# Optimization experiments

Measured on AMD Instinct MI355X. Metric: run time of the kernel, lower is better.

The kernel has to match this reference:

```python
import jax, jax.numpy as jnp
import numpy as np

COST_CLASS = 1.0
COST_POINT = 1.0


def _linear_sum_assignment(cost):
    """Pure-numpy Jonker-Volgenant / Hungarian (e-maxx formulation).
    Emulates scipy.optimize.linear_sum_assignment for a dense float cost matrix.
    Returns (row_ind, col_ind) with row_ind sorted ascending.
    """
    cost = np.asarray(cost, dtype=np.float64)
    transposed = cost.shape[0] > cost.shape[1]
    if transposed:
        cost = cost.T
    n, m = cost.shape  # n <= m
    INF = np.inf
    u = np.zeros(n + 1)
    v = np.zeros(m + 1)
    p = np.zeros(m + 1, dtype=np.int64)  # p[j] = row (1-indexed) matched to col j
    for i in range(1, n + 1):
        p[0] = i
        j0 = 0
        minv = np.full(m + 1, INF)
        way = np.zeros(m + 1, dtype=np.int64)
        used = np.zeros(m + 1, dtype=bool)
        while True:
            used[j0] = True
            i0 = p[j0]
            cur = cost[i0 - 1, :] - u[i0] - v[1:]
            free = ~used[1:]
            upd = free & (cur < minv[1:])
            minv[1:][upd] = cur[upd]
            way[1:][upd] = j0
            masked = np.where(free, minv[1:], INF)
            j1 = int(np.argmin(masked)) + 1
            delta = masked[j1 - 1]
            u[p[used]] += delta
            v[used] -= delta
            minv[1:][free] -= delta
            j0 = j1
            if p[j0] == 0:
                break
        while j0 != 0:
            j1 = way[j0]
            p[j0] = p[j1]
            j0 = j1
    ans = np.zeros(n, dtype=np.int64)  # ans[row] = col
    for j in range(1, m + 1):
        if p[j] > 0:
            ans[p[j] - 1] = j - 1
    if transposed:
        # rows of the original matrix are ans values; sort by original row index
        order = np.argsort(ans)
        return ans[order], np.arange(n, dtype=np.int64)[order]
    return np.arange(n, dtype=np.int64), ans


def _cost_matrix(pred_logits, pred_points, tgt_labels, tgt_points):
    bs, Q, C = pred_logits.shape
    T = tgt_labels.shape[1]
    out_prob = jax.nn.softmax(pred_logits.reshape(bs * Q, C), axis=-1)   # [bs*Q, C]
    out_points = pred_points.reshape(bs * Q, -1)                          # [bs*Q, 2]
    tgt_ids = tgt_labels.reshape(-1)                                      # [bs*T]
    tgt_pts = tgt_points.reshape(bs * T, -1).astype(jnp.float32)          # [bs*T, 2]
    cost_class = -out_prob[:, tgt_ids]                                    # [bs*Q, bs*T]
    # L1 cdist
    cost_point = jnp.sum(jnp.abs(out_points[:, None, :] - tgt_pts[None, :, :]), axis=-1)
    Cfull = COST_POINT * cost_point + COST_CLASS * cost_class             # [bs*Q, bs*T]
    # per-batch diagonal blocks (what the scipy split selects): [bs, Q, T]
    C4 = Cfull.reshape(bs, Q, bs, T)
    Cb = C4[jnp.arange(bs), :, jnp.arange(bs), :]
    return Cb


def setup_inputs() -> dict:
    key = jax.random.key(0)
    k1, k2, k3, k4 = jax.random.split(key, 4)
    bs, Q, C, T = 16, 1024, 92, 128
    return {
        "pred_logits": jax.random.normal(k1, (bs, Q, C), dtype=jnp.float32),
        "pred_points": jax.random.uniform(k2, (bs, Q, 2), dtype=jnp.float32),
        "tgt_labels": jax.random.randint(k3, (bs, T), 0, C, dtype=jnp.int64),
        "tgt_points": jax.random.uniform(k4, (bs, T, 2), dtype=jnp.float32),
    }


def reference(pred_logits, pred_points, tgt_labels, tgt_points):
    Cb = _cost_matrix(pred_logits, pred_points, tgt_labels, tgt_points)   # [bs, Q, T]
    Cnp = np.asarray(jax.device_get(Cb))
    rows, cols = [], []
    for b in range(Cnp.shape[0]):  # structural loop over batch for the assignment
        r, c = _linear_sum_assignment(Cnp[b])
        rows.append(r)
        cols.append(c)
    row_idx = jnp.asarray(np.stack(rows))  # [bs, T] selected query indices (sorted)
    col_idx = jnp.asarray(np.stack(cols))  # [bs, T] matched target indices
    return Cb, row_idx, col_idx
```

## Files before the change

### kernel.cpp

```cpp
#include <hip/hip_runtime.h>
#include <hip/hip_bf16.h>
#include <math.h>

#define BS 16
#define Q 1024
#define CC 92
#define T 128
#define M 1024
#define NR 128
#define NQB 16

__global__ __launch_bounds__(256) void prep_kernel(
    const float* __restrict__ logits,
    const float* __restrict__ ppts,
    const int*   __restrict__ tlab,
    const float* __restrict__ tpts,
    float* __restrict__ Cb,
    float* __restrict__ CbT,
    unsigned long long* __restrict__ part)
{
    const int blk = blockIdx.x;
    const int b   = blk & 15;
    const int qb  = blk >> 4;
    const int q0  = qb * 64;
    const int tid = threadIdx.x;
    const int lane = tid & 63;

    __shared__ float lg[64 * CC];
    __shared__ float tile[128][68];
    __shared__ float tx_sh[T], ty_sh[T];
    __shared__ int   lab_sh[T];
    __shared__ float mx_sh[64], inv_sh[64], px_sh[64], py_sh[64];

    if (tid < T) {
        lab_sh[tid] = tlab[b * T + tid];
        tx_sh[tid]  = tpts[(b * T + tid) * 2 + 0];
        ty_sh[tid]  = tpts[(b * T + tid) * 2 + 1];
    }
    if (tid < 64) {
        px_sh[tid] = ppts[((size_t)b * Q + q0 + tid) * 2 + 0];
        py_sh[tid] = ppts[((size_t)b * Q + q0 + tid) * 2 + 1];
    }
    const float* lbase = logits + ((size_t)b * Q + q0) * CC;
    for (int idx = tid; idx < 64 * CC; idx += 256) lg[idx] = lbase[idx];
    __syncthreads();

    {
        const int w = tid >> 6;
        for (int s = 0; s < 16; ++s) {
            const int ql = w * 16 + s;
            const float* c = &lg[ql * CC];
            float l0 = c[lane];
            float l1 = (lane + 64 < CC) ? c[lane + 64] : -INFINITY;
            float mx = fmaxf(l0, l1);
            #pragma unroll
            for (int off = 32; off > 0; off >>= 1)
                mx = fmaxf(mx, __shfl_down(mx, off));
            mx = __shfl(mx, 0);
            float es = expf(l0 - mx) + ((lane + 64 < CC) ? expf(l1 - mx) : 0.0f);
            #pragma unroll
            for (int off = 32; off > 0; off >>= 1) es += __shfl_down(es, off);
            es = __shfl(es, 0);
            if (lane == 0) { mx_sh[ql] = mx; inv_sh[ql] = 1.0f / es; }
        }
    }
    __syncthreads();

    {
        const int ql = tid >> 2;
        const int tc = tid & 3;
        const float px = px_sh[ql], py = py_sh[ql];
        const float mx = mx_sh[ql], inv = inv_sh[ql];
        const float* lgq = &lg[ql * CC];
        float* cbrow = Cb + ((size_t)b * Q + q0 + ql) * T + tc * 32;
        #pragma unroll
        for (int k = 0; k < 8; ++k) {
            float4 o;
            #pragma unroll
            for (int e = 0; e < 4; ++e) {
                const int t = tc * 32 + 4 * k + e;
                const int labv = lab_sh[t];
                float prob = expf(lgq[labv] - mx) * inv;
                float cp   = fabsf(px - tx_sh[t]) + fabsf(py - ty_sh[t]);
                float val  = cp - prob;
                (&o.x)[e] = val;
                tile[t][ql] = val;
            }
            ((float4*)cbrow)[k] = o;
        }
    }
    __syncthreads();

    {
        const int rg = tid >> 4;
        const int c4 = tid & 15;
        #pragma unroll
        for (int it = 0; it < 8; ++it) {
            const int t = it * 16 + rg;
            float4 v = *(const float4*)&tile[t][4 * c4];
            *(float4*)(CbT + ((size_t)b * NR + t) * Q + q0 + 4 * c4) = v;

            unsigned long long bk = ~0ull;
            const float* vf = (const float*)&v;
            #pragma unroll
            for (int e = 0; e < 4; ++e) {
                unsigned bits = __float_as_uint(vf[e]);
                unsigned mono = (bits & 0x80000000u) ? ~bits
                                                     : (bits | 0x80000000u);
                const int j = q0 + 4 * c4 + e;
                unsigned long long key =
                    ((unsigned long long)mono << 10) | (unsigned)j;
                bk = (key < bk) ? key : bk;
            }
            #pragma unroll
            for (int off = 1; off < 16; off <<= 1) {
                unsigned long long ok = __shfl_xor(bk, off);
                bk = (ok < bk) ? ok : bk;
            }
            if (c4 == 0) part[((size_t)b * NQB + qb) * NR + t] = bk;
        }
    }
}

__global__ __launch_bounds__(256) void cost_kernel(
    const float* __restrict__ logits, const float* __restrict__ ppts,
    const int* __restrict__ tlab, const float* __restrict__ tpts,
    float* __restrict__ Cb)
{
    const int blk  = blockIdx.x;
    const int b    = blk >> 8;
    const int wave = threadIdx.x >> 6;
    const int lane = threadIdx.x & 63;
    const int q    = (blk & 255) * 4 + wave;

    __shared__ float tx_sh[T], ty_sh[T];
    __shared__ int   lab_sh[T];
    __shared__ float logit_sh[4][CC];

    if (threadIdx.x < T) {
        lab_sh[threadIdx.x] = tlab[b * T + threadIdx.x];
        tx_sh[threadIdx.x]  = tpts[(b * T + threadIdx.x) * 2 + 0];
        ty_sh[threadIdx.x]  = tpts[(b * T + threadIdx.x) * 2 + 1];
    }
    const float* lrow = logits + ((size_t)b * Q + q) * CC;
    float l0 = lrow[lane];
    float l1 = (lane + 64 < CC) ? lrow[lane + 64] : -INFINITY;
    logit_sh[wave][lane] = l0;
    if (lane + 64 < CC) logit_sh[wave][lane + 64] = l1;

    float mx = fmaxf(l0, l1);
    #pragma unroll
    for (int off = 32; off > 0; off >>= 1) mx = fmaxf(mx, __shfl_down(mx, off));
    mx = __shfl(mx, 0);
    float es = expf(l0 - mx) + ((lane + 64 < CC) ? expf(l1 - mx) : 0.0f);
    #pragma unroll
    for (int off = 32; off > 0; off >>= 1) es += __shfl_down(es, off);
    es = __shfl(es, 0);
    const float inv = 1.0f / es;
    const float px = ppts[((size_t)b * Q + q) * 2 + 0];
    const float py = ppts[((size_t)b * Q + q) * 2 + 1];
    __syncthreads();
    float* outrow = Cb + ((size_t)b * Q + q) * T;
    #pragma unroll
    for (int t = lane; t < T; t += 64) {
        int   labv = lab_sh[t];
        float prob = expf(logit_sh[wave][labv] - mx) * inv;
        float cp   = fabsf(px - tx_sh[t]) + fabsf(py - ty_sh[t]);
        outrow[t]  = cp - prob;
    }
}

#define DPP_UMIN_STEP(x, ctrl)                                              \
    {                                                                       \
        unsigned _t = (unsigned)__builtin_amdgcn_update_dpp(                \
            (int)(x), (int)(x), (ctrl), 0xF, 0xF, false);                   \
        (x) = ((x) < _t) ? (x) : _t;                                        \
    }

#define DPP_UMIN_REDUCE(x)                                                  \
    DPP_UMIN_STEP(x, 0x111); DPP_UMIN_STEP(x, 0x112);                       \
    DPP_UMIN_STEP(x, 0x114); DPP_UMIN_STEP(x, 0x118);                       \
    DPP_UMIN_STEP(x, 0x142); DPP_UMIN_STEP(x, 0x143);

#define DPP_UMIN2_STEP(x1, x2, ctrl)                                        \
    {                                                                       \
        unsigned _t1 = (unsigned)__builtin_amdgcn_update_dpp(               \
            (int)(x1), (int)(x1), (ctrl), 0xF, 0xF, false);                 \
        unsigned _t2 = (unsigned)__builtin_amdgcn_update_dpp(               \
            (int)(x2), (int)(x2), (ctrl), 0xF, 0xF, false);                 \
        unsigned _hi = ((x1) > _t1) ? (x1) : _t1;                           \
        unsigned _lo2 = ((x2) < _t2) ? (x2) : _t2;                          \
        (x1) = ((x1) < _t1) ? (x1) : _t1;                                   \
        (x2) = (_hi < _lo2) ? _hi : _lo2;                                   \
    }

#define DPP_UMIN2_REDUCE(x1, x2)                                            \
    DPP_UMIN2_STEP(x1, x2, 0x111); DPP_UMIN2_STEP(x1, x2, 0x112);           \
    DPP_UMIN2_STEP(x1, x2, 0x114); DPP_UMIN2_STEP(x1, x2, 0x118);           \
    DPP_UMIN2_STEP(x1, x2, 0x142); DPP_UMIN2_STEP(x1, x2, 0x143);

__device__ __forceinline__ unsigned mono_enc(float f) {
    unsigned b = __float_as_uint(f);
    return (b & 0x80000000u) ? ~b : (b | 0x80000000u);
}
__device__ __forceinline__ float mono_dec(unsigned m) {
    unsigned b = (m & 0x80000000u) ? (m ^ 0x80000000u) : ~m;
    return __uint_as_float(b);
}

template<int USET>
__global__ __launch_bounds__(64) void solve_kernel(
    const float* __restrict__ Cb,
    const float* __restrict__ CbT,
    const unsigned long long* __restrict__ part,
    float* __restrict__ out_rows,
    float* __restrict__ out_cols)
{
    const int b    = blockIdx.x;
    const int lane = threadIdx.x;

    __shared__ int    row4col[M];
    __shared__ int    col4row[NR];
    __shared__ float  u_sh[NR];
    __shared__ int    path_lds[M];
    __shared__ int    SRr[NR];
    __shared__ float  SRd[NR];
    __shared__ int    minj_sh[NR];
    __shared__ int    claim[M];

    const float* CbB  = Cb  + (size_t)b * Q * T;
    const float* CbTB = CbT + (size_t)b * NR * Q;

    for (int j = lane; j < M;  j += 64) { row4col[j] = -1; claim[j] = 0x7fffffff; }
    for (int i = lane; i < NR; i += 64) col4row[i] = -1;

    if (part) {
        #pragma unroll
        for (int r2 = 0; r2 < 2; ++r2) {
            const int r = lane + 64 * r2;
            const unsigned long long* pr = part + (size_t)b * NQB * NR + r;
            unsigned long long k = pr[0];
            #pragma unroll
            for (int i = 1; i < NQB; ++i) {
                unsigned long long o = pr[(size_t)i * NR];
                k = (o < k) ? o : k;
            }
            minj_sh[r] = (int)(k & 1023u);
            u_sh[r] = mono_dec((unsigned)(k >> 10));
        }
    } else {
        for (int i = lane; i < NR; i += 64) { minj_sh[i] = -1; u_sh[i] = 0.0f; }
    }
    __syncthreads();

    if (part) {
        #pragma unroll
        for (int r2 = 0; r2 < 2; ++r2) {
            const int r = lane + 64 * r2;
            atomicMin(&claim[minj_sh[r]], r);
        }
        __syncthreads();
        #pragma unroll
        for (int r2 = 0; r2 < 2; ++r2) {
            const int r = lane + 64 * r2;
            const int mj = minj_sh[r];
            if (claim[mj] == r) { col4row[r] = mj; row4col[mj] = r; }
        }
        __syncthreads();
    }

    const float FINF = INFINITY;
    float v_[16], dist_[16];
    #pragma unroll
    for (int k = 0; k < 16; ++k) v_[k] = 0.0f;

    {
        unsigned long long am0 = ~__ballot(col4row[lane] >= 0);
        unsigned long long am1 = ~__ballot(col4row[lane + 64] >= 0);
        for (int half = 0; half < 2; ++half) {
            unsigned long long mask = half ? am1 : am0;
            while (mask) {
                int cur = __ffsll(mask) - 1 + 64 * half;
                mask &= mask - 1;

                for (int step = 0; step < 48; ++step) {
                    const float ucur = u_sh[cur];

                    float4 c4[4];
                    if (USET) {
                        const float4* row =
                            (const float4*)(CbTB + (size_t)cur * Q);
                        #pragma unroll
                        for (int g = 0; g < 4; ++g) c4[g] = row[lane + 64 * g];
                    } else {
                        const float* col = CbB + cur;
                        #pragma unroll
                        for (int g = 0; g < 4; ++g) {
                            float* cf = (float*)&c4[g];
                            #pragma unroll
                            for (int e = 0; e < 4; ++e)
                                cf[e] = col[(size_t)(256*g + 4*lane + e) * T];
                        }
                    }

                    float m1l = FINF, m2l = FINF; int j1l = 0;
                    #pragma unroll
                    for (int g = 0; g < 4; ++g) {
                        const float* cf = (const float*)&c4[g];
                        #pragma unroll
                        for (int e = 0; e < 4; ++e) {
                            const int k = 4 * g + e;
                            const int j = 256 * g + 4 * lane + e;
                            float r = cf[e] - ucur - v_[k];
                            if (r < m1l) { m2l = m1l; m1l = r; j1l = j; }
                            else if (r < m2l) { m2l = r; }
                        }
                    }

                    const int cand = row4col[j1l];

                    const unsigned lm1 = mono_enc(m1l);
                    unsigned e1 = lm1;
                    unsigned e2 = mono_enc(m2l);
                    DPP_UMIN2_REDUCE(e1, e2);
                    const unsigned g1 =
                        (unsigned)__builtin_amdgcn_readlane((int)e1, 63);
                    const unsigned g2 =
                        (unsigned)__builtin_amdgcn_readlane((int)e2, 63);
                    const float m1 = mono_dec(g1);
                    const float m2 = mono_dec(g2);

                    const unsigned long long bm = __ballot(lm1 == g1);
                    const int winner = __ffsll(bm) - 1;
                    const int j1   = __builtin_amdgcn_readlane(j1l, winner);
                    const int disp = __builtin_amdgcn_readlane(cand, winner);

                    if (lane == 0) u_sh[cur] = ucur + m2;
                    if (((j1 >> 2) & 63) == lane) {
                        const int k = ((j1 >> 8) << 2) | (j1 & 3);
                        v_[k] -= (m2 - m1);
                    }

                    if (lane == 0) {
                        row4col[j1]  = cur;
                        col4row[cur] = j1;
                        if (disp >= 0) col4row[disp] = -1;
                    }
                    if (disp < 0) { cur = -1; break; }
                    cur = disp;
                }
            }
        }
    }

    unsigned long long um0 = ~__ballot(col4row[lane] >= 0);
    unsigned long long um1 = ~__ballot(col4row[lane + 64] >= 0);

    for (int half = 0; half < 2; ++half) {
        unsigned long long mask = half ? um1 : um0;
        while (mask) {
            const int curRow = __ffsll(mask) - 1 + 64 * half;
            mask &= mask - 1;

            #pragma unroll
            for (int k = 0; k < 16; ++k) dist_[k] = FINF;
            unsigned used  = 0;
            float    minVal = 0.0f;
            int      i_s  = curRow;
            int      sink = -1;
            int      cnt  = 0;

            for (int guard = 0; guard <= M; ++guard) {
                const float ui = u_sh[i_s];
                const float s  = minVal - ui;

                float4 c4[4];
                if (USET) {
                    const float4* row = (const float4*)(CbTB + (size_t)i_s * Q);
                    #pragma unroll
                    for (int g = 0; g < 4; ++g) c4[g] = row[lane + 64 * g];
                } else {
                    const float* col = CbB + i_s;
                    #pragma unroll
                    for (int g = 0; g < 4; ++g) {
                        float* cf = (float*)&c4[g];
                        #pragma unroll
                        for (int e = 0; e < 4; ++e)
                            cf[e] = col[(size_t)(256 * g + 4 * lane + e) * T];
                    }
                }

                float lmin = FINF; int lidx = 0;
                #pragma unroll
                for (int g = 0; g < 4; ++g) {
                    const float* cf = (const float*)&c4[g];
                    #pragma unroll
                    for (int e = 0; e < 4; ++e) {
                        const int k = 4 * g + e;
                        const int j = 256 * g + 4 * lane + e;
                        const bool fr = ((used >> k) & 1u) == 0u;
                        float r = s + cf[e] - v_[k];
                        if (fr && r < dist_[k]) {
                            dist_[k] = r;
                            path_lds[256 * g + 64 * e + lane] = i_s;
                        }
                        float a = fr ? dist_[k] : FINF;
                        if (a < lmin) { lmin = a; lidx = j; }
                    }
                }

                const int cand = row4col[lidx];

                unsigned lmono = mono_enc(lmin);
                unsigned rmin = lmono;
                DPP_UMIN_REDUCE(rmin);
                const unsigned gmin =
                    (unsigned)__builtin_amdgcn_readlane((int)rmin, 63);

                const unsigned long long bmask = __ballot(lmono == gmin);
                const int winner = __ffsll(bmask) - 1;

                minVal = __uint_as_float(
                    (unsigned)__builtin_amdgcn_readlane(
                        (int)__float_as_uint(lmin), winner));
                const int jstar = __builtin_amdgcn_readlane(lidx, winner);

                if (((jstar >> 2) & 63) == lane)
                    used |= (1u << (((jstar >> 8) << 2) | (jstar & 3)));

                const int ra = __builtin_amdgcn_readlane(cand, winner);
                if (ra == -1) { sink = jstar; break; }
                if (lane == 0 && cnt < NR) { SRr[cnt] = ra; SRd[cnt] = minVal; }
                cnt++;
                i_s = ra;
            }

            #pragma unroll
            for (int k = 0; k < 16; ++k)
                if ((used >> k) & 1u) v_[k] += dist_[k] - minVal;

            if (lane == 0) u_sh[curRow] += minVal;
            for (int t = lane; t < cnt; t += 64)
                u_sh[SRr[t]] += minVal - SRd[t];

            if (lane == 0) {
                int j = sink;
                for (int g2 = 0; g2 < NR + 2; ++g2) {
                    int pi = path_lds[((j >> 8) << 8) | ((j & 3) << 6) |
                                      ((j >> 2) & 63)];
                    row4col[j] = pi;
                    int jn = col4row[pi];
                    col4row[pi] = j;
                    if (pi == curRow) break;
                    j = jn;
                }
            }
            __syncthreads();
        }
    }

    int base = 0;
    #pragma unroll
    for (int g = 0; g < 4; ++g) {
        int tv[4], mt[4];
        #pragma unroll
        for (int e = 0; e < 4; ++e) {
            const int j = 256 * g + 4 * lane + e;
            tv[e] = row4col[j];
            mt[e] = (tv[e] >= 0);
        }
        unsigned long long B[4];
        #pragma unroll
        for (int e = 0; e < 4; ++e) B[e] = __ballot(mt[e] != 0);
        const unsigned long long low = (1ull << lane) - 1ull;
        int below = base;
        #pragma unroll
        for (int e = 0; e < 4; ++e) below += __popcll(B[e] & low);
        int local = 0;
        #pragma unroll
        for (int e = 0; e < 4; ++e) {
            if (mt[e]) {
                const int rank = below + local;
                const int j = 256 * g + 4 * lane + e;
                out_rows[b * NR + rank] = (float)j;
                out_cols[b * NR + rank] = (float)tv[e];
                ++local;
            }
        }
        #pragma unroll
        for (int e = 0; e < 4; ++e) base += __popcll(B[e]);
    }
}

extern "C" void kernel_launch(void* const* d_in, const int* in_sizes, int n_in,
                              void* d_out, int out_size, void* d_ws, size_t ws_size,
                              hipStream_t stream) {
    const float* logits = (const float*)d_in[0];
    const float* ppts   = (const float*)d_in[1];
    const int*   tlab   = (const int*)  d_in[2];
    const float* tpts   = (const float*)d_in[3];

    float* Cb   = (float*)d_out;
    float* rows = Cb + (size_t)BS * Q * T;
    float* cols = rows + (size_t)BS * T;

    float* CbT = (float*)d_ws;
    unsigned long long* part =
        (unsigned long long*)((char*)d_ws + (size_t)BS * NR * Q * sizeof(float));

    const size_t need = (size_t)BS * NR * Q * sizeof(float)
                      + (size_t)BS * NQB * NR * sizeof(unsigned long long);

    if (ws_size >= need) {
        prep_kernel<<<BS * NQB, 256, 0, stream>>>(logits, ppts, tlab, tpts,
                                                  Cb, CbT, part);
        solve_kernel<1><<<BS, 64, 0, stream>>>(Cb, CbT, part, rows, cols);
    } else {
        cost_kernel<<<4096, 256, 0, stream>>>(logits, ppts, tlab, tpts, Cb);
        solve_kernel<0><<<BS, 64, 0, stream>>>(Cb, CbT, nullptr, rows, cols);
    }
}
```

Measured before the change: 125.9 us.

## Precompute per-row top-16 costs to shortcut auction and augmenting steps

Adds a topk_kernel that, for each transposed cost row, extracts the 16 smallest costs and a threshold tau, the 16th value with its low bits truncated. The solver mirrors column duals into LDS so that auction steps and the first Dijkstra step can use only the top-16 candidates when the second minimum provably falls below tau minus u. This avoids a full 1024-column global row scan in those cases. In exchange it adds an extra kernel launch, LDS writes of v on every dual update, and a fallback path. The bound is only correct if column duals v never go positive.

```diff
diff --git a/kernel.cpp b/kernel.cpp
--- a/kernel.cpp
+++ b/kernel.cpp
@@ -9,6 +9,7 @@
 #define M 1024
 #define NR 128
 #define NQB 16
+#define KTOP 16
 
 __global__ __launch_bounds__(256) void prep_kernel(
     const float* __restrict__ logits,
@@ -182,6 +183,10 @@
     DPP_UMIN_STEP(x, 0x114); DPP_UMIN_STEP(x, 0x118);                       \
     DPP_UMIN_STEP(x, 0x142); DPP_UMIN_STEP(x, 0x143);
 
+#define DPP_UMIN_REDUCE16(x)                                                \
+    DPP_UMIN_STEP(x, 0x111); DPP_UMIN_STEP(x, 0x112);                       \
+    DPP_UMIN_STEP(x, 0x114); DPP_UMIN_STEP(x, 0x118);
+
 #define DPP_UMIN2_STEP(x1, x2, ctrl)                                        \
     {                                                                       \
         unsigned _t1 = (unsigned)__builtin_amdgcn_update_dpp(               \
@@ -199,6 +204,10 @@
     DPP_UMIN2_STEP(x1, x2, 0x114); DPP_UMIN2_STEP(x1, x2, 0x118);           \
     DPP_UMIN2_STEP(x1, x2, 0x142); DPP_UMIN2_STEP(x1, x2, 0x143);
 
+#define DPP_UMIN2_REDUCE16(x1, x2)                                          \
+    DPP_UMIN2_STEP(x1, x2, 0x111); DPP_UMIN2_STEP(x1, x2, 0x112);           \
+    DPP_UMIN2_STEP(x1, x2, 0x114); DPP_UMIN2_STEP(x1, x2, 0x118);
+
 __device__ __forceinline__ unsigned mono_enc(float f) {
     unsigned b = __float_as_uint(f);
     return (b & 0x80000000u) ? ~b : (b | 0x80000000u);
@@ -208,11 +217,57 @@
     return __uint_as_float(b);
 }
 
+__global__ __launch_bounds__(256) void topk_kernel(
+    const float* __restrict__ CbT,
+    float2* __restrict__ topk,
+    float* __restrict__ tauv)
+{
+    const int wave = threadIdx.x >> 6;
+    const int lane = threadIdx.x & 63;
+    const int row  = blockIdx.x * 4 + wave;
+
+    const float4* rp = (const float4*)(CbT + (size_t)row * Q);
+    unsigned kk[16];
+    #pragma unroll
+    for (int g = 0; g < 4; ++g) {
+        const float4 c4 = rp[lane + 64 * g];
+        const float* cf = (const float*)&c4;
+        #pragma unroll
+        for (int e = 0; e < 4; ++e) {
+            const int j = 256 * g + 4 * lane + e;
+            kk[4 * g + e] = (mono_enc(cf[e]) & 0xFFFFFC00u) | (unsigned)j;
+        }
+    }
+
+    unsigned mykey = 0xFFFFFFFFu;
+    #pragma unroll
+    for (int r = 0; r < KTOP; ++r) {
+        unsigned lm = kk[0];
+        #pragma unroll
+        for (int e = 1; e < 16; ++e) lm = (kk[e] < lm) ? kk[e] : lm;
+        unsigned rm = lm;
+        DPP_UMIN_REDUCE(rm);
+        const unsigned g = (unsigned)__builtin_amdgcn_readlane((int)rm, 63);
+        #pragma unroll
+        for (int e = 0; e < 16; ++e) if (kk[e] == g) kk[e] = 0xFFFFFFFFu;
+        if (lane == r) mykey = g;
+    }
+
+    if (lane < KTOP) {
+        const int jj = (int)(mykey & 1023u);
+        const float c = CbT[(size_t)row * Q + jj];
+        topk[(size_t)row * KTOP + lane] = make_float2(c, __int_as_float(jj));
+    }
+    if (lane == KTOP - 1) tauv[row] = mono_dec(mykey & 0xFFFFFC00u);
+}
+
 template<int USET>
 __global__ __launch_bounds__(64) void solve_kernel(
     const float* __restrict__ Cb,
     const float* __restrict__ CbT,
     const unsigned long long* __restrict__ part,
+    const float2* __restrict__ topk,
+    const float* __restrict__ tauv,
     float* __restrict__ out_rows,
     float* __restrict__ out_cols)
 {
@@ -227,12 +282,22 @@
     __shared__ float  SRd[NR];
     __shared__ int    minj_sh[NR];
     __shared__ int    claim[M];
+    __shared__ float2 top_lds[NR * KTOP];
+    __shared__ float  v_lds[M];
+    __shared__ float  tau_lds[NR];
 
     const float* CbB  = Cb  + (size_t)b * Q * T;
     const float* CbTB = CbT + (size_t)b * NR * Q;
 
     for (int j = lane; j < M;  j += 64) { row4col[j] = -1; claim[j] = 0x7fffffff; }
     for (int i = lane; i < NR; i += 64) col4row[i] = -1;
+
+    if (USET) {
+        const float2* tsrc = topk + (size_t)b * NR * KTOP;
+        for (int i = lane; i < NR * KTOP; i += 64) top_lds[i] = tsrc[i];
+        for (int j = lane; j < M; j += 64) v_lds[j] = 0.0f;
+        for (int i = lane; i < NR; i += 64) tau_lds[i] = tauv[(size_t)b * NR + i];
+    }
 
     if (part) {
         #pragma unroll
@@ -285,60 +350,91 @@
 
                 for (int step = 0; step < 48; ++step) {
                     const float ucur = u_sh[cur];
-
-                    float4 c4[4];
+                    float m1, m2; int j1, disp;
+                    bool fast = false;
+
                     if (USET) {
-                        const float4* row =
-                            (const float4*)(CbTB + (size_t)cur * Q);
-                        #pragma unroll
-                        for (int g = 0; g < 4; ++g) c4[g] = row[lane + 64 * g];
-                    } else {
-                        const float* col = CbB + cur;
+                        const float2 te = top_lds[cur * KTOP + (lane & 15)];
+                        const int    ej = __float_as_int(te.y);
+                        const float  vv = v_lds[ej];
+                        const float  rr = (te.x - ucur) - vv;
+                        unsigned key = mono_enc(rr);
+                        if (lane >= 16) key = 0xFFFFFFFFu;
+                        const int candf = row4col[ej];
+                        unsigned e1 = key, e2 = 0xFFFFFFFFu;
+                        DPP_UMIN2_REDUCE16(e1, e2);
+                        const unsigned g1 =
+                            (unsigned)__builtin_amdgcn_readlane((int)e1, 15);
+                        const unsigned g2 =
+                            (unsigned)__builtin_amdgcn_readlane((int)e2, 15);
+                        const float lim = tau_lds[cur] - ucur;
+                        const float f2  = mono_dec(g2);
+                        if (f2 < lim) {
+                            fast = true;
+                            m1 = mono_dec(g1); m2 = f2;
+                            const unsigned long long bm = __ballot(key == g1);
+                            const int w = __ffsll(bm) - 1;
+                            j1   = __builtin_amdgcn_readlane(ej, w);
+                            disp = __builtin_amdgcn_readlane(candf, w);
+                        }
+                    }
+
+                    if (!fast) {
+                        float4 c4[4];
+                        if (USET) {
+                            const float4* row =
+                                (const float4*)(CbTB + (size_t)cur * Q);
+                            #pragma unroll
+                            for (int g = 0; g < 4; ++g) c4[g] = row[lane + 64 * g];
+                        } else {
+                            const float* col = CbB + cur;
+                            #pragma unroll
+                            for (int g = 0; g < 4; ++g) {
+                                float* cf = (float*)&c4[g];
+                                #pragma unroll
+                                for (int e = 0; e < 4; ++e)
+                                    cf[e] = col[(size_t)(256*g + 4*lane + e) * T];
+                            }
+                        }
+
+                        float m1l = FINF, m2l = FINF; int j1l = 0;
                         #pragma unroll
                         for (int g = 0; g < 4; ++g) {
-                            float* cf = (float*)&c4[g];
+                            const float* cf = (const float*)&c4[g];
                             #pragma unroll
-                            for (int e = 0; e < 4; ++e)
-                                cf[e] = col[(size_t)(256*g + 4*lane + e) * T];
+                            for (int e = 0; e < 4; ++e) {
+                                const int k = 4 * g + e;
+                                const int j = 256 * g + 4 * lane + e;
+                                float r = cf[e] - ucur - v_[k];
+                                if (r < m1l) { m2l = m1l; m1l = r; j1l = j; }
+                                else if (r < m2l) { m2l = r; }
+                            }
                         }
+
+                        const int cand = row4col[j1l];
+
+                        const unsigned lm1 = mono_enc(m1l);
+                        unsigned e1 = lm1;
+                        unsigned e2 = mono_enc(m2l);
+                        DPP_UMIN2_REDUCE(e1, e2);
+                        const unsigned g1 =
+                            (unsigned)__builtin_amdgcn_readlane((int)e1, 63);
+                        const unsigned g2 =
+                            (unsigned)__builtin_amdgcn_readlane((int)e2, 63);
+                        m1 = mono_dec(g1);
+                        m2 = mono_dec(g2);
+
+                        const unsigned long long bm = __ballot(lm1 == g1);
+                        const int winner = __ffsll(bm) - 1;
+                        j1   = __builtin_amdgcn_readlane(j1l, winner);
+                        disp = __builtin_amdgcn_readlane(cand, winner);
                     }
-
-                    float m1l = FINF, m2l = FINF; int j1l = 0;
-                    #pragma unroll
-                    for (int g = 0; g < 4; ++g) {
-                        const float* cf = (const float*)&c4[g];
-                        #pragma unroll
-                        for (int e = 0; e < 4; ++e) {
-                            const int k = 4 * g + e;
-                            const int j = 256 * g + 4 * lane + e;
-                            float r = cf[e] - ucur - v_[k];
-                            if (r < m1l) { m2l = m1l; m1l = r; j1l = j; }
-                            else if (r < m2l) { m2l = r; }
-                        }
-                    }
-
-                    const int cand = row4col[j1l];
-
-                    const unsigned lm1 = mono_enc(m1l);
-                    unsigned e1 = lm1;
-                    unsigned e2 = mono_enc(m2l);
-                    DPP_UMIN2_REDUCE(e1, e2);
-                    const unsigned g1 =
-                        (unsigned)__builtin_amdgcn_readlane((int)e1, 63);
-                    const unsigned g2 =
-                        (unsigned)__builtin_amdgcn_readlane((int)e2, 63);
-                    const float m1 = mono_dec(g1);
-                    const float m2 = mono_dec(g2);
-
-                    const unsigned long long bm = __ballot(lm1 == g1);
-                    const int winner = __ffsll(bm) - 1;
-                    const int j1   = __builtin_amdgcn_readlane(j1l, winner);
-                    const int disp = __builtin_amdgcn_readlane(cand, winner);
 
                     if (lane == 0) u_sh[cur] = ucur + m2;
                     if (((j1 >> 2) & 63) == lane) {
                         const int k = ((j1 >> 8) << 2) | (j1 & 3);
                         v_[k] -= (m2 - m1);
+                        if (USET) v_lds[j1] = v_[k];
                     }
 
                     if (lane == 0) {
@@ -361,6 +457,40 @@
         while (mask) {
             const int curRow = __ffsll(mask) - 1 + 64 * half;
             mask &= mask - 1;
+
+            bool done0 = false;
+            if (USET) {
+                const float  ui = u_sh[curRow];
+                const float  s0 = 0.0f - ui;
+                const float2 te = top_lds[curRow * KTOP + (lane & 15)];
+                const int    ej = __float_as_int(te.y);
+                const float  vv = v_lds[ej];
+                const float  rr = (s0 + te.x) - vv;
+                unsigned key = mono_enc(rr);
+                if (lane >= 16) key = 0xFFFFFFFFu;
+                const int ownf = row4col[ej];
+                unsigned rm = key;
+                DPP_UMIN_REDUCE16(rm);
+                const unsigned g =
+                    (unsigned)__builtin_amdgcn_readlane((int)rm, 15);
+                const float lim = s0 + tau_lds[curRow];
+                const float mv  = mono_dec(g);
+                if (mv < lim) {
+                    const unsigned long long bm = __ballot(key == g);
+                    const int w = __ffsll(bm) - 1;
+                    const int jstar = __builtin_amdgcn_readlane(ej, w);
+                    const int ra    = __builtin_amdgcn_readlane(ownf, w);
+                    if (ra == -1) {
+                        if (lane == 0) {
+                            u_sh[curRow]    = ui + mv;
+                            row4col[jstar]  = curRow;
+                            col4row[curRow] = jstar;
+                        }
+                        done0 = true;
+                    }
+                }
+            }
+            if (done0) { __syncthreads(); continue; }
 
             #pragma unroll
             for (int k = 0; k < 16; ++k) dist_[k] = FINF;
@@ -437,7 +567,10 @@
 
             #pragma unroll
             for (int k = 0; k < 16; ++k)
-                if ((used >> k) & 1u) v_[k] += dist_[k] - minVal;
+                if ((used >> k) & 1u) {
+                    v_[k] += dist_[k] - minVal;
+                    if (USET) v_lds[((k >> 2) << 8) + 4 * lane + (k & 3)] = v_[k];
+                }
 
             if (lane == 0) u_sh[curRow] += minVal;
             for (int t = lane; t < cnt; t += 64)
@@ -505,18 +638,26 @@
     float* cols = rows + (size_t)BS * T;
 
     float* CbT = (float*)d_ws;
-    unsigned long long* part =
-        (unsigned long long*)((char*)d_ws + (size_t)BS * NR * Q * sizeof(float));
-
-    const size_t need = (size_t)BS * NR * Q * sizeof(float)
-                      + (size_t)BS * NQB * NR * sizeof(unsigned long long);
+    const size_t cbtBytes  = (size_t)BS * NR * Q * sizeof(float);
+    const size_t partBytes = (size_t)BS * NQB * NR * sizeof(unsigned long long);
+    const size_t topkBytes = (size_t)BS * NR * KTOP * sizeof(float2);
+    const size_t tauBytes  = (size_t)BS * NR * sizeof(float);
+
+    unsigned long long* part = (unsigned long long*)((char*)d_ws + cbtBytes);
+    float2* topk = (float2*)((char*)d_ws + cbtBytes + partBytes);
+    float*  tau  = (float*) ((char*)d_ws + cbtBytes + partBytes + topkBytes);
+
+    const size_t need = cbtBytes + partBytes + topkBytes + tauBytes;
 
     if (ws_size >= need) {
         prep_kernel<<<BS * NQB, 256, 0, stream>>>(logits, ppts, tlab, tpts,
                                                   Cb, CbT, part);
-        solve_kernel<1><<<BS, 64, 0, stream>>>(Cb, CbT, part, rows, cols);
+        topk_kernel<<<BS * NR / 4, 256, 0, stream>>>(CbT, topk, tau);
+        solve_kernel<1><<<BS, 64, 0, stream>>>(Cb, CbT, part, topk, tau,
+                                               rows, cols);
     } else {
         cost_kernel<<<4096, 256, 0, stream>>>(logits, ppts, tlab, tpts, Cb);
-        solve_kernel<0><<<BS, 64, 0, stream>>>(Cb, CbT, nullptr, rows, cols);
+        solve_kernel<0><<<BS, 64, 0, stream>>>(Cb, CbT, nullptr, nullptr,
+                                               nullptr, rows, cols);
     }
 }
```

Measured after the change: 115.5 us. -8.2%, faster.
